# Performance work log

Measured on AMD Instinct MI355X. Metric: run time of the kernel, lower is better.

The kernel has to match this reference:

```python
import jax, jax.numpy as jnp
import numpy as np

NQ = 10          # qubits
NT = 32          # tokens (LCU terms)
DM = 512         # d_model
DEG = 2          # qsvt degree
B = 128          # batch
NPQC = 4 * NQ    # params per PQC application
DIM = 2 ** NQ    # statevector dimension


def ansatz14_spec(q, layers=1):
    spec = []
    for _ in range(layers):
        spec += [('ry', (i,)) for i in range(q)]
        spec += [('crx', (i, (i + 1) % q)) for i in range(q - 1, -1, -1)]
        spec += [('ry', (i,)) for i in range(q)]
        spec += [('crx', (i, (i - 1) % q)) for i in [q - 1] + list(range(q - 1))]
    return spec

SPEC = ansatz14_spec(NQ, 1)


def _gate_ry(theta):
    h = theta * 0.5
    c = jnp.cos(h)
    s = jnp.sin(h)
    m = jnp.stack([jnp.stack([c, -s], -1), jnp.stack([s, c], -1)], -2)
    return m.astype(jnp.complex64)  # (N,2,2)


def _gate_rx(theta):
    h = theta * 0.5
    c = jnp.cos(h).astype(jnp.complex64)
    s = (-1j) * jnp.sin(h).astype(jnp.complex64)
    return jnp.stack([jnp.stack([c, s], -1), jnp.stack([s, c], -1)], -2)


def _apply_1q(state, mats, wire, q):
    # state: (N, 2^q) complex; mats: (N,2,2); wire 0 is most significant bit
    N = state.shape[0]
    a = 2 ** wire
    bdim = 2 ** (q - wire - 1)
    s = state.reshape(N, a, 2, bdim)
    return jnp.einsum('nij,najb->naib', mats, s).reshape(N, 2 ** q)


def _apply_crx(state, theta, c, t, q):
    # controlled-RX: control wire c, target wire t
    N = state.shape[0]
    st = state.reshape((N,) + (2,) * q)
    ax = 1 + c
    s0 = jnp.take(st, 0, axis=ax)   # control = 0 branch: untouched
    s1 = jnp.take(st, 1, axis=ax)   # control = 1 branch: apply RX on target
    tp = t if t < c else t - 1      # target wire position after removing control axis
    s1n = _apply_1q(s1.reshape(N, -1), _gate_rx(theta), tp, q - 1).reshape(s1.shape)
    return jnp.stack([s0, s1n], axis=ax).reshape(N, 2 ** q)


def _apply_pqc(state, params, q):
    # params: (N, NPQC); fixed small gate list -> Python loop is fine
    for k, (fn, w) in enumerate(SPEC):
        th = params[:, k]
        if fn == 'ry':
            state = _apply_1q(state, _gate_ry(th), w[0], q)
        else:
            state = _apply_crx(state, th, w[0], w[1], q)
    return state


def _apply_lcu(states, params, lcu):
    # states: (B, DIM) complex; params: (B, L, NPQC); lcu: (B, L) complex
    Bn, L = lcu.shape
    rep = jnp.repeat(states, L, axis=0)                    # (B*L, DIM)
    st = _apply_pqc(rep, params.reshape(Bn * L, NPQC), NQ)
    return jnp.einsum('bld,bl->bd', st.reshape(Bn, L, DIM), lcu)


def _measure_xyz(state, q):
    # Pauli expectations per wire: order [X_0..X_{q-1}, Y_0.., Z_0..]
    N = state.shape[0]
    xs, ys, zs = [], [], []
    for w in range(q):
        s = state.reshape(N, 2 ** w, 2, -1)
        a0, a1 = s[:, :, 0, :], s[:, :, 1, :]
        cross = jnp.sum(jnp.conj(a0) * a1, axis=(1, 2))
        xs.append(2.0 * jnp.real(cross))
        ys.append(2.0 * jnp.imag(cross))
        zs.append(jnp.sum(jnp.abs(a0) ** 2 - jnp.abs(a1) ** 2, axis=(1, 2)))
    return jnp.stack(xs + ys + zs, axis=1).astype(jnp.float32)  # (B, 3q)


def reference(tokens_emb, W, b, lcu_re, lcu_im, qsvt_coeffs, ff_params):
    Bn, L, D = tokens_emb.shape
    L = min(L, NT)
    pqc_params = tokens_emb[:, :L] @ W.T + b               # (B, L, NPQC)
    lcu = (lcu_re + 1j * lcu_im).astype(jnp.complex64)[:L]
    lcu = lcu / jnp.sum(jnp.abs(lcu))
    lcu_b = jnp.broadcast_to(lcu[None], (Bn, L))
    init = jnp.zeros((Bn, DIM), jnp.complex64).at[:, 0].set(1.0)
    acc = qsvt_coeffs[0].astype(jnp.complex64) * init
    mono = init
    for k in range(1, DEG + 1):
        mono = _apply_lcu(mono, pqc_params, lcu_b)
        acc = acc + qsvt_coeffs[k].astype(jnp.complex64) * mono
    state = acc / jnp.sum(jnp.abs(qsvt_coeffs))
    state = state / jnp.linalg.norm(state, axis=-1, keepdims=True)
    ffp = jnp.broadcast_to(ff_params[None], (Bn, NPQC))
    state = _apply_pqc(state, ffp, NQ)
    return _measure_xyz(state, NQ)


def setup_inputs():
    key = jax.random.key(0)
    ks = jax.random.split(key, 7)
    return {
        'tokens_emb': jax.random.normal(ks[0], (B, NT, DM), jnp.float32),
        'W': jax.random.normal(ks[1], (NPQC, DM), jnp.float32) * 0.05,
        'b': jax.random.normal(ks[2], (NPQC,), jnp.float32),
        'lcu_re': jax.random.normal(ks[3], (NT,), jnp.float32),
        'lcu_im': jax.random.normal(ks[4], (NT,), jnp.float32),
        'qsvt_coeffs': jax.random.normal(ks[5], (DEG + 1,), jnp.float32),
        'ff_params': jax.random.normal(ks[6], (NPQC,), jnp.float32),
    }
```

## Files before the change

### kernel.cpp

```cpp
#include <hip/hip_runtime.h>
#include <hip/hip_bf16.h>


#define NQ   10
#define NT   32
#define DM   512
#define BATCH 128
#define NPQC 40
#define DIM  1024
#define NROWS (BATCH * NT)
#define PSTRIDE (BATCH * DIM)


template<int B>
__device__ __forceinline__ void g_ry(float (&ar)[16], float (&ai)[16], int lane,
                                     float c, float s) {
  static_assert(B >= 6, "RY targets must be register bits");
  constexpr int m = 1 << (B - 6);
#pragma unroll
  for (int r = 0; r < 16; ++r) {
    if (!(r & m)) {
      int r1 = r | m;
      float a0r = ar[r], a0i = ai[r], a1r = ar[r1], a1i = ai[r1];
      ar[r]  = c * a0r - s * a1r;  ai[r]  = c * a0i - s * a1i;
      ar[r1] = s * a0r + c * a1r;  ai[r1] = s * a0i + c * a1i;
    }
  }
}

template<int BC, int BT>
__device__ __forceinline__ void g_crx(float (&ar)[16], float (&ai)[16], int lane,
                                      float c, float s) {
  static_assert(BT >= 6, "CRX targets must be register bits");
  constexpr int m = 1 << (BT - 6);
  bool lane_ok = (BC >= 6) || ((lane >> BC) & 1);
#pragma unroll
  for (int r = 0; r < 16; ++r) {
    if (!(r & m)) {
      if constexpr (BC >= 6) { if (!((r >> (BC - 6)) & 1)) continue; }
      int r1 = r | m;
      float a0r = ar[r], a0i = ai[r], a1r = ar[r1], a1i = ai[r1];
      float n0r = c * a0r + s * a1i, n0i = c * a0i - s * a1r;
      float n1r = c * a1r + s * a0i, n1i = c * a1i - s * a0r;
      if (lane_ok) { ar[r] = n0r; ai[r] = n0i; ar[r1] = n1r; ai[r1] = n1i; }
    }
  }
}

template<int L0, int L1, int L2, int L3>
__device__ __forceinline__ void remap(float (&ar)[16], float (&ai)[16],
                                      float2* __restrict__ slab, int lane) {
  constexpr int LM = (1 << L0) | (1 << L1) | (1 << L2) | (1 << L3);
#pragma unroll
  for (int r = 0; r < 16; ++r) {
    int f = 0;
    if (L0 < 4 && (r & 1)) f |= 1 << L0;
    if (L1 < 4 && (r & 2)) f |= 1 << L1;
    if (L2 < 4 && (r & 4)) f |= 1 << L2;
    if (L3 < 4 && (r & 8)) f |= 1 << L3;
    slab[r * 64 + (lane ^ f)] = make_float2(ar[r], ai[r]);
  }
  asm volatile("s_waitcnt lgkmcnt(0)" ::: "memory");
  int la = lane & ~LM & 63;
  la |= ((lane >> L0) & 1) << 6;
  la |= ((lane >> L1) & 1) << 7;
  la |= ((lane >> L2) & 1) << 8;
  la |= ((lane >> L3) & 1) << 9;
  if (L0 < 4) la |= ((lane >> L0) & 1) << L0;
  if (L1 < 4) la |= ((lane >> L1) & 1) << L1;
  if (L2 < 4) la |= ((lane >> L2) & 1) << L2;
  if (L3 < 4) la |= ((lane >> L3) & 1) << L3;
#pragma unroll
  for (int r = 0; r < 16; ++r) {
    int rc = ((r & 1) ? (1 << L0) : 0) | ((r & 2) ? (1 << L1) : 0)
           | ((r & 4) ? (1 << L2) : 0) | ((r & 8) ? (1 << L3) : 0);
    float2 v = slab[la ^ rc];
    ar[r] = v.x; ai[r] = v.y;
  }
}

__device__ __forceinline__ void apply_pqc_phased(float (&ar)[16], float (&ai)[16],
    const float2* __restrict__ cs, float2* __restrict__ slab, int lane) {
  float2 t;
#define RYB(k, B)      t = cs[k]; g_ry<B>(ar, ai, lane, t.x, t.y);
#define CXB(k, BC, BT) t = cs[k]; g_crx<BC, BT>(ar, ai, lane, t.x, t.y);
  RYB(0,9) RYB(1,8) RYB(2,7) RYB(3,6)
  remap<5,4,3,2>(ar, ai, slab, lane);
  RYB(4,6) RYB(5,7) RYB(6,8) RYB(7,9)
  remap<1,0,2,3>(ar, ai, slab, lane);
  RYB(8,6) RYB(9,7)
  CXB(10,7,8) CXB(11,6,7) CXB(12,3,6)
  remap<1,0,2,3>(ar, ai, slab, lane);
  CXB(13,8,9) CXB(14,7,8) CXB(15,6,7) CXB(16,5,6)
  remap<2,3,4,5>(ar, ai, slab, lane);
  CXB(17,8,9) CXB(18,7,8) CXB(19,6,7)
  RYB(20,6) RYB(21,7) RYB(22,8) RYB(23,9)
  remap<2,3,4,5>(ar, ai, slab, lane);
  RYB(24,6) RYB(25,7) RYB(26,8) RYB(27,9)
  remap<1,0,2,3>(ar, ai, slab, lane);
  RYB(28,6) RYB(29,7)
  CXB(30,7,6) CXB(31,8,7) CXB(32,9,8) CXB(33,4,9)
  remap<4,5,1,0>(ar, ai, slab, lane);
  CXB(34,7,6) CXB(35,8,7) CXB(36,9,8) CXB(37,2,9)
  remap<2,3,4,5>(ar, ai, slab, lane);
  CXB(38,7,6) CXB(39,8,7)
#undef RYB
#undef CXB
}

__device__ __forceinline__ int p8_lane_canon(int lane) {
  return (((lane >> 1) & 1) << 9) | ((lane & 1) << 8) | (((lane >> 2) & 1) << 7)
       | (((lane >> 3) & 1) << 6) | (((lane >> 4) & 1) << 5) | (((lane >> 5) & 1) << 4);
}

__global__ __launch_bounds__(256) void params_kernel(
    const float* __restrict__ emb, const float* __restrict__ W,
    const float* __restrict__ bias,
    const float* __restrict__ lcu_re, const float* __restrict__ lcu_im,
    const float* __restrict__ ffp,
    float2* __restrict__ cs, float2* __restrict__ ffcs, float2* __restrict__ lcu) {
  int blk = blockIdx.x;
  int tid = threadIdx.x;
  if (blk == 256) {
    if (tid < NPQC) {
      float h = 0.5f * ffp[tid];
      ffcs[tid] = make_float2(cosf(h), sinf(h));
    }
    if (tid == 64) {
      float ssum = 0.f;
      for (int i = 0; i < NT; ++i) {
        float re = lcu_re[i], im = lcu_im[i];
        ssum += sqrtf(re * re + im * im);
      }
      float inv = 1.f / ssum;
      for (int i = 0; i < NT; ++i)
        lcu[i] = make_float2(lcu_re[i] * inv, lcu_im[i] * inv);
    }
    return;
  }

  __shared__ float Asl[16 * 516];
  int row0 = blk * 16;

  const float4* eg = (const float4*)(emb + (size_t)row0 * DM);
#pragma unroll
  for (int i = 0; i < 8; ++i) {
    int e = tid + i * 256;
    int r = e >> 7, k4 = e & 127;
    float4 v = eg[e];
    *(float4*)&Asl[r * 516 + k4 * 4] = v;
  }
  __syncthreads();

  int kq = tid >> 6;
  int lane = tid & 63;
  int rg = lane >> 3;
  int cg = lane & 7;

  const float* Ar0 = &Asl[(2 * rg) * 516 + kq * 128];
  const float* Ar1 = Ar0 + 516;
  const float* Bg  = W + (size_t)(5 * cg) * DM + kq * 128;

  float acc[2][5] = {};
#pragma unroll 4
  for (int k = 0; k < 128; k += 4) {
    float4 a0 = *(const float4*)(Ar0 + k);
    float4 a1 = *(const float4*)(Ar1 + k);
#pragma unroll
    for (int j = 0; j < 5; ++j) {
      float4 b = *(const float4*)(Bg + j * DM + k);
      acc[0][j] += a0.x * b.x + a0.y * b.y + a0.z * b.z + a0.w * b.w;
      acc[1][j] += a1.x * b.x + a1.y * b.y + a1.z * b.z + a1.w * b.w;
    }
  }

  __syncthreads();
  float* red = Asl;
#pragma unroll
  for (int i = 0; i < 2; ++i)
#pragma unroll
    for (int j = 0; j < 5; ++j)
      red[kq * 644 + (2 * rg + i) * 40 + 5 * cg + j] = acc[i][j];
  __syncthreads();

  for (int o = tid; o < 640; o += 256) {
    float v = bias[o % 40] + red[o] + red[644 + o] + red[1288 + o] + red[1932 + o];
    float h = 0.5f * v;
    cs[(size_t)blk * 640 + o] = make_float2(cosf(h), sinf(h));
  }
}

template<bool FIRST>
__global__ __launch_bounds__(512) void pqc_step(
    const float2* __restrict__ cs, const float2* __restrict__ lcu,
    const float2* __restrict__ src, float2* __restrict__ dst) {
  __shared__ float2 slabs[8][1024];
  int lane = threadIdx.x & 63;
  int wvu = __builtin_amdgcn_readfirstlane(threadIdx.x >> 6);
  int blk = blockIdx.x;
  int b = blk >> 2, qq = blk & 3;
  int l = qq * 8 + wvu;
  const float2* csrow = cs + (size_t)(b * NT + l) * NPQC;
  float2* slab = slabs[wvu];

  float ar[16], ai[16];
  if constexpr (FIRST) {
#pragma unroll
    for (int r = 0; r < 16; ++r) { ar[r] = 0.f; ai[r] = 0.f; }
    if (lane == 0) ar[0] = 1.f;
  } else {
    const float2* s = src + (size_t)b * DIM;
#pragma unroll
    for (int r = 0; r < 16; ++r) {
      int n = r * 64 + lane;
      float2 v0 = s[n];
      float2 v1 = s[n + PSTRIDE];
      float2 v2 = s[n + 2 * PSTRIDE];
      float2 v3 = s[n + 3 * PSTRIDE];
      ar[r] = v0.x + v1.x + v2.x + v3.x;
      ai[r] = v0.y + v1.y + v2.y + v3.y;
    }
  }

  apply_pqc_phased(ar, ai, csrow, slab, lane);

  float2 w = lcu[l];
  int pl = p8_lane_canon(lane);
  pl ^= (pl >> 5);
#pragma unroll
  for (int r = 0; r < 16; ++r) {
    int rc = ((r & 1) << 3) | ((r & 2) << 1) | ((r & 4) >> 1) | ((r & 8) >> 3);
    float cr = w.x * ar[r] - w.y * ai[r];
    float ci = w.x * ai[r] + w.y * ar[r];
    slab[pl ^ rc] = make_float2(cr, ci);
  }
  __syncthreads();

  float2* dst_b = dst + (size_t)(qq * BATCH + b) * DIM;
#pragma unroll
  for (int i = 0; i < 2; ++i) {
    int n = threadIdx.x + i * 512;
    int ph = n ^ (n >> 5);
    float sr = 0.f, si = 0.f;
#pragma unroll
    for (int s = 0; s < 8; ++s) { float2 v = slabs[s][ph]; sr += v.x; si += v.y; }
    dst_b[n] = make_float2(sr, si);
  }
}

__global__ __launch_bounds__(256) void final_kernel(
    const float2* __restrict__ part1, const float2* __restrict__ part2,
    const float* __restrict__ qsvt, const float2* __restrict__ ffcs,
    float* __restrict__ out) {
  __shared__ float2 slabs[4][1024];
  int lane = threadIdx.x & 63;
  int wvu = __builtin_amdgcn_readfirstlane(threadIdx.x >> 6);
  int b = blockIdx.x * 4 + wvu;
  float q0 = qsvt[0], q1 = qsvt[1], q2 = qsvt[2];

  float ar[16], ai[16];
  const float2* p1 = part1 + (size_t)b * DIM;
  const float2* p2 = part2 + (size_t)b * DIM;
#pragma unroll
  for (int r = 0; r < 16; ++r) {
    int n = r * 64 + lane;
    float m1r = 0.f, m1i = 0.f, m2r = 0.f, m2i = 0.f;
#pragma unroll
    for (int q = 0; q < 4; ++q) {
      float2 v1 = p1[n + q * PSTRIDE];
      float2 v2 = p2[n + q * PSTRIDE];
      m1r += v1.x; m1i += v1.y;
      m2r += v2.x; m2i += v2.y;
    }
    ar[r] = q1 * m1r + q2 * m2r;
    ai[r] = q1 * m1i + q2 * m2i;
  }
  if (lane == 0) ar[0] += q0;

  float nn = 0.f;
#pragma unroll
  for (int r = 0; r < 16; ++r) nn += ar[r] * ar[r] + ai[r] * ai[r];
#pragma unroll
  for (int o = 1; o < 64; o <<= 1) nn += __shfl_xor(nn, o);
  float inv = 1.f / sqrtf(nn);
#pragma unroll
  for (int r = 0; r < 16; ++r) { ar[r] *= inv; ai[r] *= inv; }

  apply_pqc_phased(ar, ai, ffcs, slabs[wvu], lane);

  constexpr int BPOS[10] = {1, 0, 2, 3, 4, 5, 6, 7, 8, 9};
#pragma unroll
  for (int w = 0; w < NQ; ++w) {
    const int p = BPOS[w];
    float xr = 0.f, xi = 0.f, zz = 0.f;
    if (p >= 6) {
      const int m = 1 << (p - 6);
#pragma unroll
      for (int r = 0; r < 16; ++r) {
        float mag = ar[r] * ar[r] + ai[r] * ai[r];
        zz += (r & m) ? -mag : mag;
        if (!(r & m)) {
          int r1 = r | m;
          xr += ar[r] * ar[r1] + ai[r] * ai[r1];
          xi += ar[r] * ai[r1] - ai[r] * ar[r1];
        }
      }
    } else {
      const int lm = 1 << p;
      bool lo = !(lane & lm);
#pragma unroll
      for (int r = 0; r < 16; ++r) {
        float mag = ar[r] * ar[r] + ai[r] * ai[r];
        zz += lo ? mag : -mag;
        float pr = __shfl_xor(ar[r], lm);
        float pi = __shfl_xor(ai[r], lm);
        if (lo) {
          xr += ar[r] * pr + ai[r] * pi;
          xi += ar[r] * pi - ai[r] * pr;
        }
      }
    }
#pragma unroll
    for (int o = 1; o < 64; o <<= 1) {
      xr += __shfl_xor(xr, o);
      xi += __shfl_xor(xi, o);
      zz += __shfl_xor(zz, o);
    }
    if (lane == 0) {
      out[b * 30 + w]      = 2.f * xr;
      out[b * 30 + 10 + w] = 2.f * xi;
      out[b * 30 + 20 + w] = zz;
    }
  }
}


extern "C" void kernel_launch(void* const* d_in, const int* in_sizes, int n_in,
                              void* d_out, int out_size, void* d_ws, size_t ws_size,
                              hipStream_t stream) {
  const float* emb    = (const float*)d_in[0];
  const float* W      = (const float*)d_in[1];
  const float* bias   = (const float*)d_in[2];
  const float* lcu_re = (const float*)d_in[3];
  const float* lcu_im = (const float*)d_in[4];
  const float* qsvt   = (const float*)d_in[5];
  const float* ffp    = (const float*)d_in[6];
  float* out = (float*)d_out;

  char* ws = (char*)d_ws;
  float2* cs    = (float2*)ws;
  float2* ffcs  = (float2*)(ws + 1310720);
  float2* lcu   = (float2*)(ws + 1311040);
  float2* part1 = (float2*)(ws + 1311744);
  float2* part2 = (float2*)(ws + 1311744 + 4194304);

  params_kernel<<<257, 256, 0, stream>>>(emb, W, bias, lcu_re, lcu_im, ffp,
                                         cs, ffcs, lcu);
  pqc_step<true><<<512, 512, 0, stream>>>(cs, lcu, nullptr, part1);
  pqc_step<false><<<512, 512, 0, stream>>>(cs, lcu, part1, part2);
  final_kernel<<<BATCH / 4, 256, 0, stream>>>(part1, part2, qsvt, ffcs, out);
}
```

Measured before the change: 157.5 us.

## Use packed float2 vectors for gates and shrink blocks to 4 waves

The complex amplitudes become ext_vector float2 so RY/CRX updates can be emitted as packed FMA ops. CRX masking is turned into a per-lane coefficient select instead of conditional stores. pqc_step blocks go from 8 waves to 4 and produce 8 partial sums per batch instead of 4, and final_kernel runs one wave per block. This doubles the partial-state traffic read in the next step and in final_kernel, in exchange for more, smaller blocks and cheaper arithmetic.

```diff
diff --git a/kernel.cpp b/kernel.cpp
--- a/kernel.cpp
+++ b/kernel.cpp
@@ -11,45 +11,53 @@
 #define NROWS (BATCH * NT)
 #define PSTRIDE (BATCH * DIM)
 
+typedef float v2f __attribute__((ext_vector_type(2)));
+
+__device__ __forceinline__ v2f Jrot(v2f v) {
+  return __builtin_shufflevector(v, -v, 1, 2);
+}
+__device__ __forceinline__ v2f Jc(v2f v) {
+  return __builtin_shufflevector(-v, v, 1, 2);
+}
+
 
 template<int B>
-__device__ __forceinline__ void g_ry(float (&ar)[16], float (&ai)[16], int lane,
-                                     float c, float s) {
+__device__ __forceinline__ void g_ry(v2f (&a)[16], float c, float s) {
   static_assert(B >= 6, "RY targets must be register bits");
   constexpr int m = 1 << (B - 6);
 #pragma unroll
   for (int r = 0; r < 16; ++r) {
     if (!(r & m)) {
       int r1 = r | m;
-      float a0r = ar[r], a0i = ai[r], a1r = ar[r1], a1i = ai[r1];
-      ar[r]  = c * a0r - s * a1r;  ai[r]  = c * a0i - s * a1i;
-      ar[r1] = s * a0r + c * a1r;  ai[r1] = s * a0i + c * a1i;
+      v2f a0 = a[r], a1 = a[r1];
+      a[r]  = c * a0 - s * a1;
+      a[r1] = s * a0 + c * a1;
     }
   }
 }
 
 template<int BC, int BT>
-__device__ __forceinline__ void g_crx(float (&ar)[16], float (&ai)[16], int lane,
-                                      float c, float s) {
+__device__ __forceinline__ void g_crx(v2f (&a)[16], int lane, float c, float s) {
   static_assert(BT >= 6, "CRX targets must be register bits");
   constexpr int m = 1 << (BT - 6);
   bool lane_ok = (BC >= 6) || ((lane >> BC) & 1);
+  float ce = lane_ok ? c : 1.f;
+  float se = lane_ok ? s : 0.f;
 #pragma unroll
   for (int r = 0; r < 16; ++r) {
     if (!(r & m)) {
       if constexpr (BC >= 6) { if (!((r >> (BC - 6)) & 1)) continue; }
       int r1 = r | m;
-      float a0r = ar[r], a0i = ai[r], a1r = ar[r1], a1i = ai[r1];
-      float n0r = c * a0r + s * a1i, n0i = c * a0i - s * a1r;
-      float n1r = c * a1r + s * a0i, n1i = c * a1i - s * a0r;
-      if (lane_ok) { ar[r] = n0r; ai[r] = n0i; ar[r1] = n1r; ai[r1] = n1i; }
+      v2f a0 = a[r], a1 = a[r1];
+      a[r]  = ce * a0 + se * Jrot(a1);
+      a[r1] = ce * a1 + se * Jrot(a0);
     }
   }
 }
 
 template<int L0, int L1, int L2, int L3>
-__device__ __forceinline__ void remap(float (&ar)[16], float (&ai)[16],
-                                      float2* __restrict__ slab, int lane) {
+__device__ __forceinline__ void remap(v2f (&a)[16], v2f* __restrict__ slab,
+                                      int lane) {
   constexpr int LM = (1 << L0) | (1 << L1) | (1 << L2) | (1 << L3);
 #pragma unroll
   for (int r = 0; r < 16; ++r) {
@@ -58,7 +66,7 @@
     if (L1 < 4 && (r & 2)) f |= 1 << L1;
     if (L2 < 4 && (r & 4)) f |= 1 << L2;
     if (L3 < 4 && (r & 8)) f |= 1 << L3;
-    slab[r * 64 + (lane ^ f)] = make_float2(ar[r], ai[r]);
+    slab[r * 64 + (lane ^ f)] = a[r];
   }
   asm volatile("s_waitcnt lgkmcnt(0)" ::: "memory");
   int la = lane & ~LM & 63;
@@ -74,35 +82,34 @@
   for (int r = 0; r < 16; ++r) {
     int rc = ((r & 1) ? (1 << L0) : 0) | ((r & 2) ? (1 << L1) : 0)
            | ((r & 4) ? (1 << L2) : 0) | ((r & 8) ? (1 << L3) : 0);
-    float2 v = slab[la ^ rc];
-    ar[r] = v.x; ai[r] = v.y;
-  }
-}
-
-__device__ __forceinline__ void apply_pqc_phased(float (&ar)[16], float (&ai)[16],
-    const float2* __restrict__ cs, float2* __restrict__ slab, int lane) {
+    a[r] = slab[la ^ rc];
+  }
+}
+
+__device__ __forceinline__ void apply_pqc_phased(v2f (&a)[16],
+    const float2* __restrict__ cs, v2f* __restrict__ slab, int lane) {
   float2 t;
-#define RYB(k, B)      t = cs[k]; g_ry<B>(ar, ai, lane, t.x, t.y);
-#define CXB(k, BC, BT) t = cs[k]; g_crx<BC, BT>(ar, ai, lane, t.x, t.y);
+#define RYB(k, B)      t = cs[k]; g_ry<B>(a, t.x, t.y);
+#define CXB(k, BC, BT) t = cs[k]; g_crx<BC, BT>(a, lane, t.x, t.y);
   RYB(0,9) RYB(1,8) RYB(2,7) RYB(3,6)
-  remap<5,4,3,2>(ar, ai, slab, lane);
+  remap<5,4,3,2>(a, slab, lane);
   RYB(4,6) RYB(5,7) RYB(6,8) RYB(7,9)
-  remap<1,0,2,3>(ar, ai, slab, lane);
+  remap<1,0,2,3>(a, slab, lane);
   RYB(8,6) RYB(9,7)
   CXB(10,7,8) CXB(11,6,7) CXB(12,3,6)
-  remap<1,0,2,3>(ar, ai, slab, lane);
+  remap<1,0,2,3>(a, slab, lane);
   CXB(13,8,9) CXB(14,7,8) CXB(15,6,7) CXB(16,5,6)
-  remap<2,3,4,5>(ar, ai, slab, lane);
+  remap<2,3,4,5>(a, slab, lane);
   CXB(17,8,9) CXB(18,7,8) CXB(19,6,7)
   RYB(20,6) RYB(21,7) RYB(22,8) RYB(23,9)
-  remap<2,3,4,5>(ar, ai, slab, lane);
+  remap<2,3,4,5>(a, slab, lane);
   RYB(24,6) RYB(25,7) RYB(26,8) RYB(27,9)
-  remap<1,0,2,3>(ar, ai, slab, lane);
+  remap<1,0,2,3>(a, slab, lane);
   RYB(28,6) RYB(29,7)
   CXB(30,7,6) CXB(31,8,7) CXB(32,9,8) CXB(33,4,9)
-  remap<4,5,1,0>(ar, ai, slab, lane);
+  remap<4,5,1,0>(a, slab, lane);
   CXB(34,7,6) CXB(35,8,7) CXB(36,9,8) CXB(37,2,9)
-  remap<2,3,4,5>(ar, ai, slab, lane);
+  remap<2,3,4,5>(a, slab, lane);
   CXB(38,7,6) CXB(39,8,7)
 #undef RYB
 #undef CXB
@@ -191,38 +198,36 @@
 }
 
 template<bool FIRST>
-__global__ __launch_bounds__(512) void pqc_step(
+__global__ __launch_bounds__(256) void pqc_step(
     const float2* __restrict__ cs, const float2* __restrict__ lcu,
-    const float2* __restrict__ src, float2* __restrict__ dst) {
-  __shared__ float2 slabs[8][1024];
+    const v2f* __restrict__ src, v2f* __restrict__ dst) {
+  __shared__ v2f slabs[4][1024];
   int lane = threadIdx.x & 63;
   int wvu = __builtin_amdgcn_readfirstlane(threadIdx.x >> 6);
   int blk = blockIdx.x;
-  int b = blk >> 2, qq = blk & 3;
-  int l = qq * 8 + wvu;
+  int b = blk >> 3, qq = blk & 7;
+  int l = qq * 4 + wvu;
   const float2* csrow = cs + (size_t)(b * NT + l) * NPQC;
-  float2* slab = slabs[wvu];
-
-  float ar[16], ai[16];
+  v2f* slab = slabs[wvu];
+
+  v2f a[16];
   if constexpr (FIRST) {
 #pragma unroll
-    for (int r = 0; r < 16; ++r) { ar[r] = 0.f; ai[r] = 0.f; }
-    if (lane == 0) ar[0] = 1.f;
+    for (int r = 0; r < 16; ++r) a[r] = (v2f)(0.f);
+    if (lane == 0) a[0].x = 1.f;
   } else {
-    const float2* s = src + (size_t)b * DIM;
+    const v2f* s = src + (size_t)b * DIM;
 #pragma unroll
     for (int r = 0; r < 16; ++r) {
       int n = r * 64 + lane;
-      float2 v0 = s[n];
-      float2 v1 = s[n + PSTRIDE];
-      float2 v2 = s[n + 2 * PSTRIDE];
-      float2 v3 = s[n + 3 * PSTRIDE];
-      ar[r] = v0.x + v1.x + v2.x + v3.x;
-      ai[r] = v0.y + v1.y + v2.y + v3.y;
-    }
-  }
-
-  apply_pqc_phased(ar, ai, csrow, slab, lane);
+      v2f acc = (v2f)(0.f);
+#pragma unroll
+      for (int q = 0; q < 8; ++q) acc += s[n + q * PSTRIDE];
+      a[r] = acc;
+    }
+  }
+
+  apply_pqc_phased(a, csrow, slab, lane);
 
   float2 w = lcu[l];
   int pl = p8_lane_canon(lane);
@@ -230,63 +235,57 @@
 #pragma unroll
   for (int r = 0; r < 16; ++r) {
     int rc = ((r & 1) << 3) | ((r & 2) << 1) | ((r & 4) >> 1) | ((r & 8) >> 3);
-    float cr = w.x * ar[r] - w.y * ai[r];
-    float ci = w.x * ai[r] + w.y * ar[r];
-    slab[pl ^ rc] = make_float2(cr, ci);
+    slab[pl ^ rc] = w.x * a[r] + w.y * Jc(a[r]);
   }
   __syncthreads();
 
-  float2* dst_b = dst + (size_t)(qq * BATCH + b) * DIM;
-#pragma unroll
-  for (int i = 0; i < 2; ++i) {
-    int n = threadIdx.x + i * 512;
+  v2f* dst_b = dst + (size_t)(qq * BATCH + b) * DIM;
+#pragma unroll
+  for (int i = 0; i < 4; ++i) {
+    int n = threadIdx.x + i * 256;
     int ph = n ^ (n >> 5);
-    float sr = 0.f, si = 0.f;
-#pragma unroll
-    for (int s = 0; s < 8; ++s) { float2 v = slabs[s][ph]; sr += v.x; si += v.y; }
-    dst_b[n] = make_float2(sr, si);
-  }
-}
-
-__global__ __launch_bounds__(256) void final_kernel(
-    const float2* __restrict__ part1, const float2* __restrict__ part2,
+    v2f sum = (v2f)(0.f);
+#pragma unroll
+    for (int s = 0; s < 4; ++s) sum += slabs[s][ph];
+    dst_b[n] = sum;
+  }
+}
+
+__global__ __launch_bounds__(64) void final_kernel(
+    const v2f* __restrict__ part1, const v2f* __restrict__ part2,
     const float* __restrict__ qsvt, const float2* __restrict__ ffcs,
     float* __restrict__ out) {
-  __shared__ float2 slabs[4][1024];
-  int lane = threadIdx.x & 63;
-  int wvu = __builtin_amdgcn_readfirstlane(threadIdx.x >> 6);
-  int b = blockIdx.x * 4 + wvu;
+  __shared__ v2f slab[1024];
+  int lane = threadIdx.x;
+  int b = blockIdx.x;
   float q0 = qsvt[0], q1 = qsvt[1], q2 = qsvt[2];
 
-  float ar[16], ai[16];
-  const float2* p1 = part1 + (size_t)b * DIM;
-  const float2* p2 = part2 + (size_t)b * DIM;
+  v2f a[16];
+  const v2f* p1 = part1 + (size_t)b * DIM;
+  const v2f* p2 = part2 + (size_t)b * DIM;
 #pragma unroll
   for (int r = 0; r < 16; ++r) {
     int n = r * 64 + lane;
-    float m1r = 0.f, m1i = 0.f, m2r = 0.f, m2i = 0.f;
-#pragma unroll
-    for (int q = 0; q < 4; ++q) {
-      float2 v1 = p1[n + q * PSTRIDE];
-      float2 v2 = p2[n + q * PSTRIDE];
-      m1r += v1.x; m1i += v1.y;
-      m2r += v2.x; m2i += v2.y;
-    }
-    ar[r] = q1 * m1r + q2 * m2r;
-    ai[r] = q1 * m1i + q2 * m2i;
-  }
-  if (lane == 0) ar[0] += q0;
+    v2f m1 = (v2f)(0.f), m2 = (v2f)(0.f);
+#pragma unroll
+    for (int q = 0; q < 8; ++q) {
+      m1 += p1[n + q * PSTRIDE];
+      m2 += p2[n + q * PSTRIDE];
+    }
+    a[r] = q1 * m1 + q2 * m2;
+  }
+  if (lane == 0) a[0].x += q0;
 
   float nn = 0.f;
 #pragma unroll
-  for (int r = 0; r < 16; ++r) nn += ar[r] * ar[r] + ai[r] * ai[r];
+  for (int r = 0; r < 16; ++r) nn += a[r].x * a[r].x + a[r].y * a[r].y;
 #pragma unroll
   for (int o = 1; o < 64; o <<= 1) nn += __shfl_xor(nn, o);
   float inv = 1.f / sqrtf(nn);
 #pragma unroll
-  for (int r = 0; r < 16; ++r) { ar[r] *= inv; ai[r] *= inv; }
-
-  apply_pqc_phased(ar, ai, ffcs, slabs[wvu], lane);
+  for (int r = 0; r < 16; ++r) a[r] *= inv;
+
+  apply_pqc_phased(a, ffcs, slab, lane);
 
   constexpr int BPOS[10] = {1, 0, 2, 3, 4, 5, 6, 7, 8, 9};
 #pragma unroll
@@ -297,12 +296,12 @@
       const int m = 1 << (p - 6);
 #pragma unroll
       for (int r = 0; r < 16; ++r) {
-        float mag = ar[r] * ar[r] + ai[r] * ai[r];
+        float mag = a[r].x * a[r].x + a[r].y * a[r].y;
         zz += (r & m) ? -mag : mag;
         if (!(r & m)) {
           int r1 = r | m;
-          xr += ar[r] * ar[r1] + ai[r] * ai[r1];
-          xi += ar[r] * ai[r1] - ai[r] * ar[r1];
+          xr += a[r].x * a[r1].x + a[r].y * a[r1].y;
+          xi += a[r].x * a[r1].y - a[r].y * a[r1].x;
         }
       }
     } else {
@@ -310,13 +309,13 @@
       bool lo = !(lane & lm);
 #pragma unroll
       for (int r = 0; r < 16; ++r) {
-        float mag = ar[r] * ar[r] + ai[r] * ai[r];
+        float mag = a[r].x * a[r].x + a[r].y * a[r].y;
         zz += lo ? mag : -mag;
-        float pr = __shfl_xor(ar[r], lm);
-        float pi = __shfl_xor(ai[r], lm);
+        float pr = __shfl_xor(a[r].x, lm);
+        float pi = __shfl_xor(a[r].y, lm);
         if (lo) {
-          xr += ar[r] * pr + ai[r] * pi;
-          xi += ar[r] * pi - ai[r] * pr;
+          xr += a[r].x * pr + a[r].y * pi;
+          xi += a[r].x * pi - a[r].y * pr;
         }
       }
     }
@@ -351,12 +350,12 @@
   float2* cs    = (float2*)ws;
   float2* ffcs  = (float2*)(ws + 1310720);
   float2* lcu   = (float2*)(ws + 1311040);
-  float2* part1 = (float2*)(ws + 1311744);
-  float2* part2 = (float2*)(ws + 1311744 + 4194304);
+  v2f*    part1 = (v2f*)(ws + 1311744);
+  v2f*    part2 = (v2f*)(ws + 1311744 + 8388608);
 
   params_kernel<<<257, 256, 0, stream>>>(emb, W, bias, lcu_re, lcu_im, ffp,
                                          cs, ffcs, lcu);
-  pqc_step<true><<<512, 512, 0, stream>>>(cs, lcu, nullptr, part1);
-  pqc_step<false><<<512, 512, 0, stream>>>(cs, lcu, part1, part2);
-  final_kernel<<<BATCH / 4, 256, 0, stream>>>(part1, part2, qsvt, ffcs, out);
-}
+  pqc_step<true><<<1024, 256, 0, stream>>>(cs, lcu, nullptr, part1);
+  pqc_step<false><<<1024, 256, 0, stream>>>(cs, lcu, part1, part2);
+  final_kernel<<<BATCH, 64, 0, stream>>>(part1, part2, qsvt, ffcs, out);
+}
```

New measurement: 201.6 us. 27.9% more time.
